# Performance work log

Measured on AMD Instinct MI355X. Metric: run time of the kernel, lower is better.

The kernel has to match this reference:

```python
import jax, jax.numpy as jnp
import numpy as np

N_NODES = 100000
N_EDGES = 1000000
IN_FEATS = 128
HID = 128
OUT_FEATS = 64


def _glorot(key, shape):
    fan_in, fan_out = shape
    lim = (6.0 / (fan_in + fan_out)) ** 0.5
    return jax.random.uniform(key, shape, jnp.float32, -lim, lim)


def setup_inputs() -> dict:
    key = jax.random.key(0)
    ks = jax.random.split(key, 12)
    x = jax.random.normal(ks[0], (N_NODES, IN_FEATS), jnp.float32)
    src = jax.random.randint(ks[1], (N_EDGES,), 0, N_NODES, jnp.int32)
    dst = jax.random.randint(ks[2], (N_EDGES,), 0, N_NODES, jnp.int32)
    return {
        "x": x, "src": src, "dst": dst,
        "w_self0": _glorot(ks[3], (IN_FEATS, HID)),
        "w_neigh0": _glorot(ks[4], (IN_FEATS, HID)),
        "b0": jnp.zeros((HID,), jnp.float32),
        "w_self1": _glorot(ks[5], (HID, HID)),
        "w_neigh1": _glorot(ks[6], (HID, HID)),
        "b1": jnp.zeros((HID,), jnp.float32),
        "w_self2": _glorot(ks[7], (HID, OUT_FEATS)),
        "w_neigh2": _glorot(ks[8], (HID, OUT_FEATS)),
        "b2": jnp.zeros((OUT_FEATS,), jnp.float32),
    }


def _sage_conv(x, src, dst, deg_inv, w_self, w_neigh, b):
    # irregular gather over neighbors, then mean segment-reduce onto dst
    neigh_sum = jax.ops.segment_sum(x[src], dst, num_segments=x.shape[0])  # [N, d]
    neigh_mean = neigh_sum * deg_inv  # zero-in-degree nodes -> 0
    return x @ w_self + neigh_mean @ w_neigh + b


def reference(x, src, dst,
              w_self0, w_neigh0, b0,
              w_self1, w_neigh1, b1,
              w_self2, w_neigh2, b2):
    n = x.shape[0]
    deg = jax.ops.segment_sum(jnp.ones_like(dst, jnp.float32), dst, num_segments=n)
    deg_inv = jnp.where(deg > 0, 1.0 / jnp.maximum(deg, 1.0), 0.0)[:, None]  # [N,1]
    h = _sage_conv(x, src, dst, deg_inv, w_self0, w_neigh0, b0)
    h = jax.nn.relu(h)  # dropout is identity in eval
    h = _sage_conv(h, src, dst, deg_inv, w_self1, w_neigh1, b1)
    h = jax.nn.relu(h)
    h = _sage_conv(h, src, dst, deg_inv, w_self2, w_neigh2, b2)
    return h
```

## Files before the change

kernel.cpp:

```cpp
#include <hip/hip_runtime.h>
#include <stdint.h>

#define N_NODES 100000
#define N_EDGES 1000000
#define NB 782
#define CAP 4096
#define EPB 2048
#define SCB ((N_EDGES + EPB - 1) / EPB)
#define PREPB 6410

typedef __attribute__((ext_vector_type(2))) _Float16 f16x2;
typedef __attribute__((ext_vector_type(8))) _Float16 f16x8;
typedef __attribute__((ext_vector_type(4))) float f32x4;

__device__ __forceinline__ unsigned short f2h(float f) {
  _Float16 h = (_Float16)f;
  return *(unsigned short*)&h;
}

__global__ void k_scatter_prep(const int* __restrict__ src, const int* __restrict__ dst,
                               int* __restrict__ bcnt, unsigned int* __restrict__ stage,
                               const float* __restrict__ x, unsigned short* __restrict__ xb,
                               const float* __restrict__ ws0, const float* __restrict__ wn0,
                               unsigned short* __restrict__ wt0,
                               const float* __restrict__ ws1, const float* __restrict__ wn1,
                               unsigned short* __restrict__ wt1,
                               const float* __restrict__ ws2, const float* __restrict__ wn2,
                               unsigned short* __restrict__ wt2) {
  __shared__ int h[NB];
  __shared__ int cur[NB];
  int t = threadIdx.x;
  if (blockIdx.x < SCB) {
    for (int i = t; i < NB; i += 256) h[i] = 0;
    __syncthreads();
    int base = blockIdx.x * EPB;
#pragma unroll 8
    for (int k = 0; k < EPB / 256; k++) {
      int i = base + t + k * 256;
      if (i < N_EDGES) atomicAdd(&h[dst[i] >> 7], 1);
    }
    __syncthreads();
    for (int i = t; i < NB; i += 256) {
      int c = h[i];
      cur[i] = c ? atomicAdd(&bcnt[i], c) : 0;
    }
    __syncthreads();
#pragma unroll 8
    for (int k = 0; k < EPB / 256; k++) {
      int i = base + t + k * 256;
      if (i < N_EDGES) {
        int d = dst[i];
        int b = d >> 7;
        int pos = atomicAdd(&cur[b], 1);
        stage[(size_t)b * CAP + pos] = ((unsigned int)(d & 127) << 17) | (unsigned int)src[i];
      }
    }
    return;
  }
  int b = blockIdx.x - SCB;
  if (b < 6250) {
    int i = b * 256 + t;
    float4 a = ((const float4*)x)[2 * i];
    float4 v = ((const float4*)x)[2 * i + 1];
    unsigned short r[8] = {f2h(a.x), f2h(a.y), f2h(a.z), f2h(a.w),
                           f2h(v.x), f2h(v.y), f2h(v.z), f2h(v.w)};
    *(uint4*)(xb + (size_t)i * 8) = *(uint4*)r;
    return;
  }
  int w = (b - 6250) * 256 + t;
  const float* WS; const float* WN; unsigned short* WT; int nout;
  if (w < 16384) { WS = ws0; WN = wn0; WT = wt0; nout = 128; }
  else if (w < 32768) { w -= 16384; WS = ws1; WN = wn1; WT = wt1; nout = 128; }
  else { w -= 32768; if (w >= 8192) return; WS = ws2; WN = wn2; WT = wt2; nout = 64; }
  int n = w >> 7, k = w & 127;
  WT[n * 256 + k] = f2h(WS[(size_t)k * nout + n]);
  WT[n * 256 + 128 + k] = f2h(WN[(size_t)k * nout + n]);
}

__global__ void k_bucket(const unsigned int* __restrict__ stage, const int* __restrict__ bcnt,
                         int* __restrict__ csr, int* __restrict__ rowbeg,
                         int* __restrict__ rowend, float* __restrict__ dinv) {
  __shared__ int cnt[128], sc[128], cur[128];
  int b = blockIdx.x, t = threadIdx.x;
  int nb = bcnt[b];
  const unsigned int* sb = stage + (size_t)b * CAP;
  int e0 = b * CAP;
  if (t < 128) cnt[t] = 0;
  __syncthreads();
  for (int e = t; e < nb; e += 256)
    atomicAdd(&cnt[sb[e] >> 17], 1);
  __syncthreads();
  int myc = (t < 128) ? cnt[t] : 0;
  if (t < 128) sc[t] = myc;
  __syncthreads();
  for (int off = 1; off < 128; off <<= 1) {
    int a = (t < 128 && t >= off) ? sc[t - off] : 0;
    __syncthreads();
    if (t < 128) sc[t] += a;
    __syncthreads();
  }
  if (t < 128) {
    int node = b * 128 + t;
    int ex = sc[t] - myc;
    cur[t] = ex;
    if (node < N_NODES) {
      rowbeg[node] = e0 + ex;
      rowend[node] = e0 + ex + myc;
      dinv[node] = myc ? 1.0f / (float)myc : 0.0f;
    }
  }
  __syncthreads();
  for (int e = t; e < nb; e += 256) {
    unsigned int v = sb[e];
    int l = v >> 17;
    int pos = e0 + atomicAdd(&cur[l], 1);
    csr[pos] = (int)(v & 0x1FFFFu);
  }
}

__global__ void k_agg(const unsigned short* __restrict__ feat,
                      const int* __restrict__ rowbeg, const int* __restrict__ rowend,
                      const int* __restrict__ csr,
                      const float* __restrict__ dinv, unsigned short* __restrict__ nm) {
  int wv = threadIdx.x >> 6, lane = threadIdx.x & 63;
  int node = blockIdx.x * 4 + wv;
  if (node >= N_NODES) return;
  const uint4* fp = (const uint4*)feat;
  int s0 = rowbeg[node], s1 = rowend[node];
  int g = lane >> 4, c = lane & 15;
  f16x2 q0 = {0, 0}, q1 = {0, 0}, q2 = {0, 0}, q3 = {0, 0};
  for (int j = s0 + g; j < s1; j += 16) {
    int i1 = j + 4, i2 = j + 8, i3 = j + 12;
    bool h1 = i1 < s1, h2 = i2 < s1, h3 = i3 < s1;
    int c0 = csr[j];
    int c1 = h1 ? csr[i1] : 0;
    int c2 = h2 ? csr[i2] : 0;
    int c3 = h3 ? csr[i3] : 0;
    uint4 v0, v1, v2, v3;
    v0 = fp[(size_t)c0 * 16 + c];
    if (h1) v1 = fp[(size_t)c1 * 16 + c];
    if (h2) v2 = fp[(size_t)c2 * 16 + c];
    if (h3) v3 = fp[(size_t)c3 * 16 + c];
    q0 += *(const f16x2*)&v0.x; q1 += *(const f16x2*)&v0.y;
    q2 += *(const f16x2*)&v0.z; q3 += *(const f16x2*)&v0.w;
    if (h1) {
      q0 += *(const f16x2*)&v1.x; q1 += *(const f16x2*)&v1.y;
      q2 += *(const f16x2*)&v1.z; q3 += *(const f16x2*)&v1.w;
    }
    if (h2) {
      q0 += *(const f16x2*)&v2.x; q1 += *(const f16x2*)&v2.y;
      q2 += *(const f16x2*)&v2.z; q3 += *(const f16x2*)&v2.w;
    }
    if (h3) {
      q0 += *(const f16x2*)&v3.x; q1 += *(const f16x2*)&v3.y;
      q2 += *(const f16x2*)&v3.z; q3 += *(const f16x2*)&v3.w;
    }
  }
  float a0 = (float)q0[0], a1 = (float)q0[1], a2 = (float)q1[0], a3 = (float)q1[1];
  float a4 = (float)q2[0], a5 = (float)q2[1], a6 = (float)q3[0], a7 = (float)q3[1];
#define RED(x) x += __shfl_xor(x, 16); x += __shfl_xor(x, 32);
  RED(a0) RED(a1) RED(a2) RED(a3) RED(a4) RED(a5) RED(a6) RED(a7)
#undef RED
  if (g == 0) {
    float di = dinv[node];
    uint4 o;
    o.x = ((unsigned int)f2h(a1 * di) << 16) | (unsigned int)f2h(a0 * di);
    o.y = ((unsigned int)f2h(a3 * di) << 16) | (unsigned int)f2h(a2 * di);
    o.z = ((unsigned int)f2h(a5 * di) << 16) | (unsigned int)f2h(a4 * di);
    o.w = ((unsigned int)f2h(a7 * di) << 16) | (unsigned int)f2h(a6 * di);
    ((uint4*)(nm + (size_t)node * 128))[c] = o;
  }
}

template <int NOUT, bool RELU, bool OUT_F16>
__global__ __launch_bounds__(256, 4) void k_mm(
    const unsigned short* __restrict__ A0, const unsigned short* __restrict__ A1,
    const unsigned short* __restrict__ WT, const float* __restrict__ Bv,
    void* __restrict__ OUT) {
  constexpr int NFC = NOUT / 64;
  __shared__ __align__(16) unsigned short sm[16896];
  const int row0 = blockIdx.x * 64;
  const int tid = threadIdx.x;

  for (int i = tid; i < 1024; i += 256) {
    int r = i >> 4, c = i & 15;
    int gr = row0 + r;
    if (gr >= N_NODES) gr = N_NODES - 1;
    *(uint4*)(sm + r * 264 + c * 8) = ((const uint4*)(A0 + (size_t)gr * 128))[c];
    *(uint4*)(sm + r * 264 + 128 + c * 8) = ((const uint4*)(A1 + (size_t)gr * 128))[c];
  }

  const int lane = tid & 63;
  const int w = tid >> 6;
  const int r16 = lane & 15;
  const int kg = lane >> 4;
  const int wc0 = w * (NOUT / 4);

  f32x4 acc[4][NFC];
#pragma unroll
  for (int rf = 0; rf < 4; rf++)
#pragma unroll
    for (int cf = 0; cf < NFC; cf++) acc[rf][cf] = (f32x4){0.f, 0.f, 0.f, 0.f};

  __syncthreads();

  const unsigned short* wtb = WT + (size_t)(wc0 + r16) * 256 + kg * 8;
  const unsigned short* asb = sm + r16 * 264 + kg * 8;

  for (int ks = 0; ks < 8; ks++) {
    f16x8 a[4];
#pragma unroll
    for (int rf = 0; rf < 4; rf++)
      a[rf] = *(const f16x8*)(asb + rf * 16 * 264 + ks * 32);
#pragma unroll
    for (int cf = 0; cf < NFC; cf++) {
      f16x8 b = *(const f16x8*)(wtb + cf * 16 * 256 + ks * 32);
#pragma unroll
      for (int rf = 0; rf < 4; rf++)
        acc[rf][cf] = __builtin_amdgcn_mfma_f32_16x16x32_f16(a[rf], b, acc[rf][cf], 0, 0, 0);
    }
  }

  __syncthreads();

  if (OUT_F16) {
    constexpr int LSO = NOUT + 8;
    unsigned short* so = sm;
#pragma unroll
    for (int rf = 0; rf < 4; rf++)
#pragma unroll
      for (int cf = 0; cf < NFC; cf++) {
        int col = wc0 + cf * 16 + r16;
        float bias = Bv[col];
#pragma unroll
        for (int r = 0; r < 4; r++) {
          int row = rf * 16 + kg * 4 + r;
          float v = acc[rf][cf][r] + bias;
          if (RELU) v = fmaxf(v, 0.f);
          so[row * LSO + col] = f2h(v);
        }
      }
    __syncthreads();
    unsigned short* O = (unsigned short*)OUT;
    for (int i = tid; i < 64 * (NOUT / 8); i += 256) {
      int r = i / (NOUT / 8), c = i % (NOUT / 8);
      int gr = row0 + r;
      if (gr < N_NODES)
        *(uint4*)(O + (size_t)gr * NOUT + c * 8) = *(const uint4*)(so + r * LSO + c * 8);
    }
  } else {
    constexpr int LSO = NOUT + 4;
    float* so = (float*)sm;
#pragma unroll
    for (int rf = 0; rf < 4; rf++)
#pragma unroll
      for (int cf = 0; cf < NFC; cf++) {
        int col = wc0 + cf * 16 + r16;
        float bias = Bv[col];
#pragma unroll
        for (int r = 0; r < 4; r++) {
          int row = rf * 16 + kg * 4 + r;
          float v = acc[rf][cf][r] + bias;
          if (RELU) v = fmaxf(v, 0.f);
          so[row * LSO + col] = v;
        }
      }
    __syncthreads();
    float* O = (float*)OUT;
    for (int i = tid; i < 64 * (NOUT / 4); i += 256) {
      int r = i / (NOUT / 4), c = i % (NOUT / 4);
      int gr = row0 + r;
      if (gr < N_NODES)
        *(float4*)(O + (size_t)gr * NOUT + c * 4) = *(const float4*)(so + r * LSO + c * 4);
    }
  }
}


extern "C" void kernel_launch(void* const* d_in, const int* in_sizes, int n_in,
                              void* d_out, int out_size, void* d_ws, size_t ws_size,
                              hipStream_t stream) {
  const float* x   = (const float*)d_in[0];
  const int*   src = (const int*)d_in[1];
  const int*   dst = (const int*)d_in[2];
  const float* ws0 = (const float*)d_in[3];
  const float* wn0 = (const float*)d_in[4];
  const float* b0  = (const float*)d_in[5];
  const float* ws1 = (const float*)d_in[6];
  const float* wn1 = (const float*)d_in[7];
  const float* b1  = (const float*)d_in[8];
  const float* ws2 = (const float*)d_in[9];
  const float* wn2 = (const float*)d_in[10];
  const float* b2  = (const float*)d_in[11];
  float* out = (float*)d_out;

  uint8_t* base = (uint8_t*)d_ws;
  size_t off = 0;
  auto alloc = [&](size_t bytes) -> void* {
    void* p = base + off;
    off = (off + bytes + 255) & ~(size_t)255;
    return p;
  };
  int*   rowbeg  = (int*)alloc((size_t)N_NODES * 4);
  int*   rowend  = (int*)alloc((size_t)N_NODES * 4);
  float* dinv    = (float*)alloc((size_t)N_NODES * 4);
  int*   csr     = (int*)alloc((size_t)NB * CAP * 4);
  unsigned int* stage = (unsigned int*)alloc((size_t)NB * CAP * 4);
  int*   bcnt    = (int*)alloc((size_t)NB * 4);
  unsigned short* xb  = (unsigned short*)alloc((size_t)N_NODES * 128 * 2);
  unsigned short* nmb = (unsigned short*)alloc((size_t)N_NODES * 128 * 2);
  unsigned short* h1b = (unsigned short*)alloc((size_t)N_NODES * 128 * 2);
  unsigned short* h2b = (unsigned short*)alloc((size_t)N_NODES * 128 * 2);
  unsigned short* wt0 = (unsigned short*)alloc(128 * 256 * 2);
  unsigned short* wt1 = (unsigned short*)alloc(128 * 256 * 2);
  unsigned short* wt2 = (unsigned short*)alloc(64 * 256 * 2);

  hipMemsetAsync(bcnt, 0, (size_t)NB * 4, stream);
  k_scatter_prep<<<SCB + PREPB, 256, 0, stream>>>(src, dst, bcnt, stage,
                                                  x, xb, ws0, wn0, wt0,
                                                  ws1, wn1, wt1, ws2, wn2, wt2);
  k_bucket<<<NB, 256, 0, stream>>>(stage, bcnt, csr, rowbeg, rowend, dinv);

  const int GMM = (N_NODES + 63) / 64;

  k_agg<<<25000, 256, 0, stream>>>(xb, rowbeg, rowend, csr, dinv, nmb);
  k_mm<128, true, true><<<GMM, 256, 0, stream>>>(xb, nmb, wt0, b0, h1b);
  k_agg<<<25000, 256, 0, stream>>>(h1b, rowbeg, rowend, csr, dinv, nmb);
  k_mm<128, true, true><<<GMM, 256, 0, stream>>>(h1b, nmb, wt1, b1, h2b);
  k_agg<<<25000, 256, 0, stream>>>(h2b, rowbeg, rowend, csr, dinv, nmb);
  k_mm<64, false, false><<<GMM, 256, 0, stream>>>(h2b, nmb, wt2, b2, out);
}
```

Baseline: 246.9 us.

## Reorder last SAGE layer to project before aggregating, halving gathered feature width

For the final layer, the code now multiplies h2 by the stacked [w_self2 | w_neigh2] first. That yields a float self term plus a 64-wide fp16 neighbour projection, which is then mean-aggregated over edges and added to the self term. This uses linearity of the mean to gather 64 instead of 128 features per edge in the last aggregation and drops one matmul pass over the aggregated buffer. It adds an fp32 self-term buffer write and read, and changes fp16 rounding order. The scatter edges-per-block is also halved to launch more, smaller scatter blocks.

```diff
diff --git a/kernel.cpp b/kernel.cpp
--- a/kernel.cpp
+++ b/kernel.cpp
@@ -5,9 +5,9 @@
 #define N_EDGES 1000000
 #define NB 782
 #define CAP 4096
-#define EPB 2048
+#define EPB 1024
 #define SCB ((N_EDGES + EPB - 1) / EPB)
-#define PREPB 6410
+#define PREPB 6442
 
 typedef __attribute__((ext_vector_type(2))) _Float16 f16x2;
 typedef __attribute__((ext_vector_type(8))) _Float16 f16x8;
@@ -34,7 +34,7 @@
     for (int i = t; i < NB; i += 256) h[i] = 0;
     __syncthreads();
     int base = blockIdx.x * EPB;
-#pragma unroll 8
+#pragma unroll 4
     for (int k = 0; k < EPB / 256; k++) {
       int i = base + t + k * 256;
       if (i < N_EDGES) atomicAdd(&h[dst[i] >> 7], 1);
@@ -45,7 +45,7 @@
       cur[i] = c ? atomicAdd(&bcnt[i], c) : 0;
     }
     __syncthreads();
-#pragma unroll 8
+#pragma unroll 4
     for (int k = 0; k < EPB / 256; k++) {
       int i = base + t + k * 256;
       if (i < N_EDGES) {
@@ -68,13 +68,21 @@
     return;
   }
   int w = (b - 6250) * 256 + t;
-  const float* WS; const float* WN; unsigned short* WT; int nout;
-  if (w < 16384) { WS = ws0; WN = wn0; WT = wt0; nout = 128; }
-  else if (w < 32768) { w -= 16384; WS = ws1; WN = wn1; WT = wt1; nout = 128; }
-  else { w -= 32768; if (w >= 8192) return; WS = ws2; WN = wn2; WT = wt2; nout = 64; }
-  int n = w >> 7, k = w & 127;
-  WT[n * 256 + k] = f2h(WS[(size_t)k * nout + n]);
-  WT[n * 256 + 128 + k] = f2h(WN[(size_t)k * nout + n]);
+  if (w < 16384) {
+    int n = w >> 7, k = w & 127;
+    wt0[n * 256 + k] = f2h(ws0[(size_t)k * 128 + n]);
+    wt0[n * 256 + 128 + k] = f2h(wn0[(size_t)k * 128 + n]);
+  } else if (w < 32768) {
+    w -= 16384;
+    int n = w >> 7, k = w & 127;
+    wt1[n * 256 + k] = f2h(ws1[(size_t)k * 128 + n]);
+    wt1[n * 256 + 128 + k] = f2h(wn1[(size_t)k * 128 + n]);
+  } else {
+    w -= 32768;
+    int n = w >> 7, k = w & 127;
+    float v = (n < 64) ? ws2[(size_t)k * 64 + n] : wn2[(size_t)k * 64 + (n - 64)];
+    wt2[n * 128 + k] = f2h(v);
+  }
 }
 
 __global__ void k_bucket(const unsigned int* __restrict__ stage, const int* __restrict__ bcnt,
@@ -172,11 +180,66 @@
   }
 }
 
-template <int NOUT, bool RELU, bool OUT_F16>
+__global__ void k_agg2(const unsigned short* __restrict__ zn,
+                       const int* __restrict__ rowbeg, const int* __restrict__ rowend,
+                       const int* __restrict__ csr, const float* __restrict__ dinv,
+                       const float* __restrict__ self2, float* __restrict__ out) {
+  int wv = threadIdx.x >> 6, lane = threadIdx.x & 63;
+  int node = blockIdx.x * 4 + wv;
+  if (node >= N_NODES) return;
+  const uint4* fp = (const uint4*)zn;
+  int s0 = rowbeg[node], s1 = rowend[node];
+  int g = lane >> 3, c = lane & 7;
+  f16x2 q0 = {0, 0}, q1 = {0, 0}, q2 = {0, 0}, q3 = {0, 0};
+  for (int j = s0 + g; j < s1; j += 32) {
+    int i1 = j + 8, i2 = j + 16, i3 = j + 24;
+    bool h1 = i1 < s1, h2 = i2 < s1, h3 = i3 < s1;
+    int c0 = csr[j];
+    int c1 = h1 ? csr[i1] : 0;
+    int c2 = h2 ? csr[i2] : 0;
+    int c3 = h3 ? csr[i3] : 0;
+    uint4 v0, v1, v2, v3;
+    v0 = fp[(size_t)c0 * 8 + c];
+    if (h1) v1 = fp[(size_t)c1 * 8 + c];
+    if (h2) v2 = fp[(size_t)c2 * 8 + c];
+    if (h3) v3 = fp[(size_t)c3 * 8 + c];
+    q0 += *(const f16x2*)&v0.x; q1 += *(const f16x2*)&v0.y;
+    q2 += *(const f16x2*)&v0.z; q3 += *(const f16x2*)&v0.w;
+    if (h1) {
+      q0 += *(const f16x2*)&v1.x; q1 += *(const f16x2*)&v1.y;
+      q2 += *(const f16x2*)&v1.z; q3 += *(const f16x2*)&v1.w;
+    }
+    if (h2) {
+      q0 += *(const f16x2*)&v2.x; q1 += *(const f16x2*)&v2.y;
+      q2 += *(const f16x2*)&v2.z; q3 += *(const f16x2*)&v2.w;
+    }
+    if (h3) {
+      q0 += *(const f16x2*)&v3.x; q1 += *(const f16x2*)&v3.y;
+      q2 += *(const f16x2*)&v3.z; q3 += *(const f16x2*)&v3.w;
+    }
+  }
+  float a0 = (float)q0[0], a1 = (float)q0[1], a2 = (float)q1[0], a3 = (float)q1[1];
+  float a4 = (float)q2[0], a5 = (float)q2[1], a6 = (float)q3[0], a7 = (float)q3[1];
+#define RED8(x) x += __shfl_xor(x, 8); x += __shfl_xor(x, 16); x += __shfl_xor(x, 32);
+  RED8(a0) RED8(a1) RED8(a2) RED8(a3) RED8(a4) RED8(a5) RED8(a6) RED8(a7)
+#undef RED8
+  if (g == 0) {
+    float di = dinv[node];
+    const float4* sp = (const float4*)(self2 + (size_t)node * 64);
+    float4 s0v = sp[c * 2], s1v = sp[c * 2 + 1];
+    float4 o0 = {s0v.x + a0 * di, s0v.y + a1 * di, s0v.z + a2 * di, s0v.w + a3 * di};
+    float4 o1 = {s1v.x + a4 * di, s1v.y + a5 * di, s1v.z + a6 * di, s1v.w + a7 * di};
+    float4* op = (float4*)(out + (size_t)node * 64);
+    op[c * 2] = o0;
+    op[c * 2 + 1] = o1;
+  }
+}
+
+template <int NOUT, bool RELU>
 __global__ __launch_bounds__(256, 4) void k_mm(
     const unsigned short* __restrict__ A0, const unsigned short* __restrict__ A1,
     const unsigned short* __restrict__ WT, const float* __restrict__ Bv,
-    void* __restrict__ OUT) {
+    unsigned short* __restrict__ OUT) {
   constexpr int NFC = NOUT / 64;
   __shared__ __align__(16) unsigned short sm[16896];
   const int row0 = blockIdx.x * 64;
@@ -223,56 +286,123 @@
 
   __syncthreads();
 
-  if (OUT_F16) {
-    constexpr int LSO = NOUT + 8;
-    unsigned short* so = sm;
+  constexpr int LSO = NOUT + 8;
+  unsigned short* so = sm;
+#pragma unroll
+  for (int rf = 0; rf < 4; rf++)
+#pragma unroll
+    for (int cf = 0; cf < NFC; cf++) {
+      int col = wc0 + cf * 16 + r16;
+      float bias = Bv[col];
+#pragma unroll
+      for (int r = 0; r < 4; r++) {
+        int row = rf * 16 + kg * 4 + r;
+        float v = acc[rf][cf][r] + bias;
+        if (RELU) v = fmaxf(v, 0.f);
+        so[row * LSO + col] = f2h(v);
+      }
+    }
+  __syncthreads();
+  for (int i = tid; i < 64 * (NOUT / 8); i += 256) {
+    int r = i / (NOUT / 8), c = i % (NOUT / 8);
+    int gr = row0 + r;
+    if (gr < N_NODES)
+      *(uint4*)(OUT + (size_t)gr * NOUT + c * 8) = *(const uint4*)(so + r * LSO + c * 8);
+  }
+}
+
+__global__ __launch_bounds__(256, 4) void k_mm2(
+    const unsigned short* __restrict__ A, const unsigned short* __restrict__ WT,
+    const float* __restrict__ Bv, float* __restrict__ SELF,
+    unsigned short* __restrict__ ZN) {
+  __shared__ __align__(16) unsigned short sm[64 * 136];
+  const int row0 = blockIdx.x * 64;
+  const int tid = threadIdx.x;
+
+  for (int i = tid; i < 1024; i += 256) {
+    int r = i >> 4, c = i & 15;
+    int gr = row0 + r;
+    if (gr >= N_NODES) gr = N_NODES - 1;
+    *(uint4*)(sm + r * 136 + c * 8) = ((const uint4*)(A + (size_t)gr * 128))[c];
+  }
+
+  const int lane = tid & 63;
+  const int w = tid >> 6;
+  const int r16 = lane & 15;
+  const int kg = lane >> 4;
+  const int wc0 = w * 32;
+
+  f32x4 acc[4][2];
+#pragma unroll
+  for (int rf = 0; rf < 4; rf++)
+#pragma unroll
+    for (int cf = 0; cf < 2; cf++) acc[rf][cf] = (f32x4){0.f, 0.f, 0.f, 0.f};
+
+  __syncthreads();
+
+  const unsigned short* wtb = WT + (size_t)(wc0 + r16) * 128 + kg * 8;
+  const unsigned short* asb = sm + r16 * 136 + kg * 8;
+
+  for (int ks = 0; ks < 4; ks++) {
+    f16x8 a[4];
 #pragma unroll
     for (int rf = 0; rf < 4; rf++)
-#pragma unroll
-      for (int cf = 0; cf < NFC; cf++) {
-        int col = wc0 + cf * 16 + r16;
+      a[rf] = *(const f16x8*)(asb + rf * 16 * 136 + ks * 32);
+#pragma unroll
+    for (int cf = 0; cf < 2; cf++) {
+      f16x8 b = *(const f16x8*)(wtb + cf * 16 * 128 + ks * 32);
+#pragma unroll
+      for (int rf = 0; rf < 4; rf++)
+        acc[rf][cf] = __builtin_amdgcn_mfma_f32_16x16x32_f16(a[rf], b, acc[rf][cf], 0, 0, 0);
+    }
+  }
+
+  __syncthreads();
+
+  float* sof = (float*)sm;
+#pragma unroll
+  for (int rf = 0; rf < 4; rf++)
+#pragma unroll
+    for (int cf = 0; cf < 2; cf++) {
+      int col = wc0 + cf * 16 + r16;
+      if (col < 64) {
         float bias = Bv[col];
 #pragma unroll
         for (int r = 0; r < 4; r++) {
           int row = rf * 16 + kg * 4 + r;
-          float v = acc[rf][cf][r] + bias;
-          if (RELU) v = fmaxf(v, 0.f);
-          so[row * LSO + col] = f2h(v);
+          sof[row * 68 + col] = acc[rf][cf][r] + bias;
         }
       }
-    __syncthreads();
-    unsigned short* O = (unsigned short*)OUT;
-    for (int i = tid; i < 64 * (NOUT / 8); i += 256) {
-      int r = i / (NOUT / 8), c = i % (NOUT / 8);
-      int gr = row0 + r;
-      if (gr < N_NODES)
-        *(uint4*)(O + (size_t)gr * NOUT + c * 8) = *(const uint4*)(so + r * LSO + c * 8);
-    }
-  } else {
-    constexpr int LSO = NOUT + 4;
-    float* so = (float*)sm;
-#pragma unroll
-    for (int rf = 0; rf < 4; rf++)
-#pragma unroll
-      for (int cf = 0; cf < NFC; cf++) {
-        int col = wc0 + cf * 16 + r16;
-        float bias = Bv[col];
+    }
+  __syncthreads();
+  for (int i = tid; i < 1024; i += 256) {
+    int r = i >> 4, c = i & 15;
+    int gr = row0 + r;
+    if (gr < N_NODES)
+      *(float4*)(SELF + (size_t)gr * 64 + c * 4) = *(const float4*)(sof + r * 68 + c * 4);
+  }
+  __syncthreads();
+
+  unsigned short* soh = sm;
+#pragma unroll
+  for (int rf = 0; rf < 4; rf++)
+#pragma unroll
+    for (int cf = 0; cf < 2; cf++) {
+      int col = wc0 + cf * 16 + r16;
+      if (col >= 64) {
 #pragma unroll
         for (int r = 0; r < 4; r++) {
           int row = rf * 16 + kg * 4 + r;
-          float v = acc[rf][cf][r] + bias;
-          if (RELU) v = fmaxf(v, 0.f);
-          so[row * LSO + col] = v;
+          soh[row * 72 + (col - 64)] = f2h(acc[rf][cf][r]);
         }
       }
-    __syncthreads();
-    float* O = (float*)OUT;
-    for (int i = tid; i < 64 * (NOUT / 4); i += 256) {
-      int r = i / (NOUT / 4), c = i % (NOUT / 4);
-      int gr = row0 + r;
-      if (gr < N_NODES)
-        *(float4*)(O + (size_t)gr * NOUT + c * 4) = *(const float4*)(so + r * LSO + c * 4);
-    }
+    }
+  __syncthreads();
+  for (int i = tid; i < 512; i += 256) {
+    int r = i >> 3, c = i & 7;
+    int gr = row0 + r;
+    if (gr < N_NODES)
+      *(uint4*)(ZN + (size_t)gr * 64 + c * 8) = *(const uint4*)(soh + r * 72 + c * 8);
   }
 }
 
@@ -311,9 +441,11 @@
   unsigned short* nmb = (unsigned short*)alloc((size_t)N_NODES * 128 * 2);
   unsigned short* h1b = (unsigned short*)alloc((size_t)N_NODES * 128 * 2);
   unsigned short* h2b = (unsigned short*)alloc((size_t)N_NODES * 128 * 2);
+  float* self2 = (float*)alloc((size_t)N_NODES * 64 * 4);
+  unsigned short* znb = (unsigned short*)alloc((size_t)N_NODES * 64 * 2);
   unsigned short* wt0 = (unsigned short*)alloc(128 * 256 * 2);
   unsigned short* wt1 = (unsigned short*)alloc(128 * 256 * 2);
-  unsigned short* wt2 = (unsigned short*)alloc(64 * 256 * 2);
+  unsigned short* wt2 = (unsigned short*)alloc(128 * 128 * 2);
 
   hipMemsetAsync(bcnt, 0, (size_t)NB * 4, stream);
   k_scatter_prep<<<SCB + PREPB, 256, 0, stream>>>(src, dst, bcnt, stage,
@@ -324,9 +456,9 @@
   const int GMM = (N_NODES + 63) / 64;
 
   k_agg<<<25000, 256, 0, stream>>>(xb, rowbeg, rowend, csr, dinv, nmb);
-  k_mm<128, true, true><<<GMM, 256, 0, stream>>>(xb, nmb, wt0, b0, h1b);
+  k_mm<128, true><<<GMM, 256, 0, stream>>>(xb, nmb, wt0, b0, h1b);
   k_agg<<<25000, 256, 0, stream>>>(h1b, rowbeg, rowend, csr, dinv, nmb);
-  k_mm<128, true, true><<<GMM, 256, 0, stream>>>(h1b, nmb, wt1, b1, h2b);
-  k_agg<<<25000, 256, 0, stream>>>(h2b, rowbeg, rowend, csr, dinv, nmb);
-  k_mm<64, false, false><<<GMM, 256, 0, stream>>>(h2b, nmb, wt2, b2, out);
-}
+  k_mm<128, true><<<GMM, 256, 0, stream>>>(h1b, nmb, wt1, b1, h2b);
+  k_mm2<<<GMM, 256, 0, stream>>>(h2b, wt2, b2, self2, znb);
+  k_agg2<<<25000, 256, 0, stream>>>(znb, rowbeg, rowend, csr, dinv, self2, out);
+}
```

Result: slower. 257.2 us (+4.2%).
